# Performance work log

Hardware: AMD Instinct MI355X
Metric: run time of the kernel (lower is better)

## Reference

```python
import jax, jax.numpy as jnp
import numpy as np

TOPK = 8
EXTRA = 0  # ADDITIONAL_LAYERS_IN_GPU
CPU_TOPK = int(0.25 * 64)  # CPU_MOE_RATIO * num_experts = 16


def setup_inputs() -> dict:
    key = jax.random.key(0)
    k1, k2 = jax.random.split(key)
    hidden_states = jax.random.normal(k1, (4, 4096, 4096), dtype=jnp.float32)
    wg_weight = jax.random.normal(k2, (64, 4096), dtype=jnp.float32) * 0.02
    return {"hidden_states": hidden_states, "wg_weight": wg_weight}


def reference(hidden_states, wg_weight):
    bsz, seq_len, hidden_size = hidden_states.shape
    x = hidden_states.reshape(-1, hidden_size).astype(jnp.float32)  # [T, H]
    logits = jnp.einsum('th,eh->te', x, wg_weight)  # [T, 64]
    gates = jax.nn.softmax(logits, axis=1)
    values_all, indices_all = jax.lax.top_k(gates, TOPK + EXTRA)
    expert_weight = values_all[:, :TOPK]
    expert_index = indices_all[:, :TOPK]
    _, cpu_expert_index = jax.lax.top_k(gates, CPU_TOPK)
    cpu_expert_index = cpu_expert_index[:, 8 + EXTRA:]
    # norm_topk_prob=True, topk > 1
    eps = jnp.finfo(jnp.float32).eps
    denom = jnp.maximum(expert_weight.sum(axis=1, keepdims=True), eps)
    expert_weight = expert_weight / denom
    return (expert_weight, expert_index, cpu_expert_index, indices_all)
```

## Files before the change

### kernel.cpp

```cpp
#include <hip/hip_runtime.h>

#define T_TOK 16384
#define HDIM  4096
#define NEXP  64
#define TAU   2e-4f
#define BM    128

typedef unsigned short u16;
typedef u16   u16x8  __attribute__((ext_vector_type(8)));
typedef __bf16 bf16x8 __attribute__((ext_vector_type(8)));
typedef float f32x4  __attribute__((ext_vector_type(4)));

__device__ __forceinline__ void gld16(const void* g, void* l) {
    __builtin_amdgcn_global_load_lds(
        (const __attribute__((address_space(1))) void*)g,
        (__attribute__((address_space(3))) void*)l, 16, 0, 0);
}

__global__ __launch_bounds__(256)
void wsplit_kernel(const float* __restrict__ w, u16x8* __restrict__ wfrag,
                   float4* __restrict__ wt4, int* __restrict__ counter) {
    if (blockIdx.x == 0 && threadIdx.x == 0) counter[0] = 0;

    const int id  = blockIdx.x * 256 + threadIdx.x;
    const int e   = id >> 9;
    const int k8g = id & 511;
    const int k   = k8g * 8;

    const float* wp = w + (size_t)e * HDIM + k;
    const float4 v0 = *(const float4*)wp;
    const float4 v1 = *(const float4*)(wp + 4);

    wt4[(size_t)(2 * k8g) * NEXP + e]     = v0;
    wt4[(size_t)(2 * k8g + 1) * NEXP + e] = v1;

    const float fv[8] = {v0.x, v0.y, v0.z, v0.w, v1.x, v1.y, v1.z, v1.w};
    bf16x8 hv, lv;
#pragma unroll
    for (int j = 0; j < 8; ++j) {
        const __bf16 h = (__bf16)fv[j];
        hv[j] = h;
        lv[j] = (__bf16)(fv[j] - (float)h);
    }
    const int chunk = k >> 6;
    const int k8 = (k >> 3) & 7, ks = k8 >> 2, g = k8 & 3, nt = e >> 4;
    const int U = ks * 256 + nt * 64 + 16 * g + (e & 15);
    wfrag[(size_t)chunk * 1024 + U]       = __builtin_bit_cast(u16x8, hv);
    wfrag[(size_t)chunk * 1024 + 512 + U] = __builtin_bit_cast(u16x8, lv);
}

__global__ __launch_bounds__(256, 3)
void gate_gemm_mfma(const float* __restrict__ x, const u16x8* __restrict__ wfrag,
                    float* __restrict__ partial, int ksplit) {
    const int b      = blockIdx.x;
    const int kslice = b % ksplit;
    const int tblk   = b / ksplit;
    const int kspan  = HDIM / ksplit;
    const int k0     = kslice * kspan;
    const int t0     = tblk * BM;
    const int nch    = kspan >> 5;

    __shared__ __align__(16) unsigned char smem[48 * 1024];

    const int tid  = threadIdx.x;
    const int lane = tid & 63;
    const int wv   = tid >> 6;

    f32x4 acc[2][4];
#pragma unroll
    for (int m = 0; m < 2; ++m)
#pragma unroll
        for (int nt = 0; nt < 4; ++nt) acc[m][nt] = (f32x4){0.f, 0.f, 0.f, 0.f};

    auto stage = [&](int c, int p) {
        const int kc  = k0 + (c << 5);
        const u16x8* wsrc = wfrag + (size_t)(kc >> 6) * 1024 + ((c & 1) << 8);
        unsigned char* base = smem + (size_t)p * 1536 * 16;
        gld16(wsrc + tid,       base + (size_t)tid * 16);
        gld16(wsrc + 512 + tid, base + (size_t)(256 + tid) * 16);
#pragma unroll
        for (int j = 0; j < 4; ++j) {
            const int u   = tid + 256 * j;
            const int row = u >> 3;
            const int k4l = (u & 7) ^ (row & 7);
            gld16(x + (size_t)(t0 + row) * HDIM + kc + 4 * k4l,
                  base + (size_t)(512 + u) * 16);
        }
    };

    stage(0, 0);
    stage(1, 1);

    for (int c = 0; c < nch; ++c) {
        const int p = c & 1;

        if (c + 1 < nch) asm volatile("s_waitcnt vmcnt(6)" ::: "memory");
        else             asm volatile("s_waitcnt vmcnt(0)" ::: "memory");
        __builtin_amdgcn_sched_barrier(0);
        __builtin_amdgcn_s_barrier();
        __builtin_amdgcn_sched_barrier(0);

        const u16x8* wb = (const u16x8*)(smem + (size_t)p * 1536 * 16);
        const float* xb = (const float*)(smem + ((size_t)p * 1536 + 512) * 16);
        const int k8 = lane >> 4;

        bf16x8 axh[2], axl[2];
#pragma unroll
        for (int m = 0; m < 2; ++m) {
            const int row = (wv * 2 + m) * 16 + (lane & 15);
            const int p0  = row * 8 + ((2 * k8)     ^ (row & 7));
            const int p1  = row * 8 + ((2 * k8 + 1) ^ (row & 7));
            const float4 va = *(const float4*)(xb + 4 * p0);
            const float4 vb = *(const float4*)(xb + 4 * p1);
            const float fv[8] = {va.x, va.y, va.z, va.w, vb.x, vb.y, vb.z, vb.w};
            bf16x8 hv, lv;
#pragma unroll
            for (int j = 0; j < 8; ++j) {
                const __bf16 h = (__bf16)fv[j];
                hv[j] = h;
                lv[j] = (__bf16)(fv[j] - (float)h);
            }
            axh[m] = hv;
            axl[m] = lv;
        }
#pragma unroll
        for (int nt = 0; nt < 4; ++nt) {
            const bf16x8 bh = __builtin_bit_cast(bf16x8, wb[nt * 64 + lane]);
            const bf16x8 bl = __builtin_bit_cast(bf16x8, wb[256 + nt * 64 + lane]);
#pragma unroll
            for (int m = 0; m < 2; ++m) {
                acc[m][nt] = __builtin_amdgcn_mfma_f32_16x16x32_bf16(axh[m], bh, acc[m][nt], 0, 0, 0);
                acc[m][nt] = __builtin_amdgcn_mfma_f32_16x16x32_bf16(axh[m], bl, acc[m][nt], 0, 0, 0);
                acc[m][nt] = __builtin_amdgcn_mfma_f32_16x16x32_bf16(axl[m], bh, acc[m][nt], 0, 0, 0);
            }
        }

        __builtin_amdgcn_sched_barrier(0);
        __builtin_amdgcn_s_barrier();
        __builtin_amdgcn_sched_barrier(0);
        if (c + 2 < nch) stage(c + 2, p);
    }

    float* op = partial + (size_t)kslice * T_TOK * NEXP;
    const int ecol = lane & 15;
#pragma unroll
    for (int m = 0; m < 2; ++m) {
        const int trow = t0 + (wv * 2 + m) * 16 + ((lane >> 4) << 2);
#pragma unroll
        for (int nt = 0; nt < 4; ++nt)
#pragma unroll
            for (int r = 0; r < 4; ++r)
                op[(size_t)(trow + r) * NEXP + nt * 16 + ecol] = acc[m][nt][r];
    }
}

__global__ __launch_bounds__(256)
void gate_topk_f32(const float* __restrict__ partial, int ksplit,
                   float* __restrict__ out, int* __restrict__ list,
                   int* __restrict__ counter) {
    const int wave = threadIdx.x >> 6;
    const int lane = threadIdx.x & 63;
    const int t = blockIdx.x * 4 + wave;

    float l = 0.f;
    for (int s = 0; s < ksplit; ++s)
        l += partial[(size_t)s * T_TOK * NEXP + (size_t)t * NEXP + lane];

    float v = l;
    const int idx = lane;
    float myval = -3.4e38f;
    int   myidx = 0;
#pragma unroll
    for (int r = 0; r < 17; ++r) {
        float bv = v;
        int   bi = idx;
#pragma unroll
        for (int s = 1; s < 64; s <<= 1) {
            const float ov = __shfl_xor(bv, s);
            const int   oi = __shfl_xor(bi, s);
            if (ov > bv || (ov == bv && oi < bi)) { bv = ov; bi = oi; }
        }
        if (lane == r) { myval = bv; myidx = bi; }
        if (idx == bi) v = -3.4e38f;
    }

    const float nxt = __shfl(myval, (lane + 1) & 63);
    const bool close = (lane < 16) && (myval - nxt < TAU);
    if (__ballot(close) != 0ull) {
        if (lane == 0) { const int p = atomicAdd(counter, 1); list[p] = t; }
    }

    const float m = __shfl(myval, 0);
    const float p = (lane < 16) ? expf(myval - m) : 0.f;
    float s8 = (lane < 8) ? p : 0.f;
#pragma unroll
    for (int s = 1; s < 64; s <<= 1) s8 += __shfl_xor(s8, s);

    float* ew = out;
    float* ei = out + (size_t)T_TOK * 8;
    float* ci = out + (size_t)2 * T_TOK * 8;
    float* ia = out + (size_t)3 * T_TOK * 8;
    if (lane < 8) {
        ew[(size_t)t * 8 + lane] = p / s8;
        ei[(size_t)t * 8 + lane] = (float)myidx;
        ia[(size_t)t * 8 + lane] = (float)myidx;
    } else if (lane < 16) {
        ci[(size_t)t * 8 + (lane - 8)] = (float)myidx;
    }
}

__global__ __launch_bounds__(256)
void repair_partial(const float* __restrict__ x, const float4* __restrict__ wt4,
                    const int* __restrict__ list, const int* __restrict__ counter,
                    double* __restrict__ fpart) {
    const int lane = threadIdx.x & 63;
    const int wid  = (int)((blockIdx.x * blockDim.x + threadIdx.x) >> 6);
    const int nw   = (int)((gridDim.x * blockDim.x) >> 6);
    const int nit  = counter[0] * 16;

    for (int it = wid; it < nit; it += nw) {
        const int li = it >> 4;
        const int ks = it & 15;
        const int t  = __builtin_amdgcn_readfirstlane(list[li]);
        const float4* xr4 = (const float4*)(x + (size_t)t * HDIM) + ks * 64;
        const float4* wb  = wt4 + (size_t)ks * 64 * NEXP;

        double a0 = 0.0, a1 = 0.0, a2 = 0.0, a3 = 0.0;
#pragma unroll 4
        for (int j = 0; j < 64; j += 4) {
            const float4 w0 = wb[(size_t)(j + 0) * NEXP + lane];
            const float4 w1 = wb[(size_t)(j + 1) * NEXP + lane];
            const float4 w2 = wb[(size_t)(j + 2) * NEXP + lane];
            const float4 w3 = wb[(size_t)(j + 3) * NEXP + lane];
            const float4 x0 = xr4[j + 0];
            const float4 x1 = xr4[j + 1];
            const float4 x2 = xr4[j + 2];
            const float4 x3 = xr4[j + 3];
            a0 = fma((double)x0.x, (double)w0.x, a0);
            a0 = fma((double)x0.y, (double)w0.y, a0);
            a0 = fma((double)x0.z, (double)w0.z, a0);
            a0 = fma((double)x0.w, (double)w0.w, a0);
            a1 = fma((double)x1.x, (double)w1.x, a1);
            a1 = fma((double)x1.y, (double)w1.y, a1);
            a1 = fma((double)x1.z, (double)w1.z, a1);
            a1 = fma((double)x1.w, (double)w1.w, a1);
            a2 = fma((double)x2.x, (double)w2.x, a2);
            a2 = fma((double)x2.y, (double)w2.y, a2);
            a2 = fma((double)x2.z, (double)w2.z, a2);
            a2 = fma((double)x2.w, (double)w2.w, a2);
            a3 = fma((double)x3.x, (double)w3.x, a3);
            a3 = fma((double)x3.y, (double)w3.y, a3);
            a3 = fma((double)x3.z, (double)w3.z, a3);
            a3 = fma((double)x3.w, (double)w3.w, a3);
        }
        fpart[(size_t)li * 1024 + ks * 64 + lane] = (a0 + a1) + (a2 + a3);
    }
}

__global__ __launch_bounds__(256)
void repair_final(const double* __restrict__ fpart, const int* __restrict__ list,
                  const int* __restrict__ counter, float* __restrict__ out) {
    const int lane = threadIdx.x & 63;
    const int wid  = (int)((blockIdx.x * blockDim.x + threadIdx.x) >> 6);
    const int nw   = (int)((gridDim.x * blockDim.x) >> 6);
    const int n    = counter[0];

    for (int li = wid; li < n; li += nw) {
        const int t = __builtin_amdgcn_readfirstlane(list[li]);

        double v = 0.0;
#pragma unroll
        for (int ks = 0; ks < 16; ++ks)
            v += fpart[(size_t)li * 1024 + ks * 64 + lane];

        const int idx = lane;
        double mylog = -1.0e308;
        int    myidx = 0;
#pragma unroll
        for (int r = 0; r < 16; ++r) {
            double bv = v;
            int    bi = idx;
#pragma unroll
            for (int s = 1; s < 64; s <<= 1) {
                const double ov = __shfl_xor(bv, s);
                const int    oi = __shfl_xor(bi, s);
                if (ov > bv || (ov == bv && oi < bi)) { bv = ov; bi = oi; }
            }
            if (lane == r) { mylog = bv; myidx = bi; }
            if (idx == bi) v = -1.0e308;
        }

        const double m = __shfl(mylog, 0);
        const float p = (lane < 16) ? expf((float)(mylog - m)) : 0.f;
        float s8 = (lane < 8) ? p : 0.f;
#pragma unroll
        for (int s = 1; s < 64; s <<= 1) s8 += __shfl_xor(s8, s);

        float* ew = out;
        float* ei = out + (size_t)T_TOK * 8;
        float* ci = out + (size_t)2 * T_TOK * 8;
        float* ia = out + (size_t)3 * T_TOK * 8;
        if (lane < 8) {
            ew[(size_t)t * 8 + lane] = p / s8;
            ei[(size_t)t * 8 + lane] = (float)myidx;
            ia[(size_t)t * 8 + lane] = (float)myidx;
        } else if (lane < 16) {
            ci[(size_t)t * 8 + (lane - 8)] = (float)myidx;
        }
    }
}

extern "C" void kernel_launch(void* const* d_in, const int* in_sizes, int n_in,
                              void* d_out, int out_size, void* d_ws, size_t ws_size,
                              hipStream_t stream) {
    const float* x = (const float*)d_in[0];
    const float* w = (const float*)d_in[1];
    float* out     = (float*)d_out;

    const size_t slice      = (size_t)T_TOK * NEXP * sizeof(float);
    const size_t wfragBytes = (size_t)64 * 1024 * 16;
    const size_t wt4Bytes   = (size_t)NEXP * HDIM * sizeof(float);
    const size_t fpartBytes = (size_t)T_TOK * 16 * NEXP * sizeof(double);
    const size_t extra      = wfragBytes + wt4Bytes + fpartBytes +
                              (size_t)T_TOK * sizeof(int) + 64;

    int ksplit = 1;
    if      (ws_size >= 4 * slice + extra) ksplit = 4;
    else if (ws_size >= 2 * slice + extra) ksplit = 2;

    float*  partial = (float*)d_ws;
    u16x8*  wfrag   = (u16x8*)((char*)d_ws + (size_t)ksplit * slice);
    float4* wt4     = (float4*)((char*)wfrag + wfragBytes);
    double* fpart   = (double*)((char*)wt4 + wt4Bytes);
    int*    list    = (int*)((char*)fpart + fpartBytes);
    int*    counter = list + T_TOK;

    wsplit_kernel<<<128, 256, 0, stream>>>(w, wfrag, wt4, counter);
    gate_gemm_mfma<<<ksplit * (T_TOK / BM), 256, 0, stream>>>(x, wfrag, partial, ksplit);
    gate_topk_f32<<<T_TOK / 4, 256, 0, stream>>>(partial, ksplit, out, list, counter);
    repair_partial<<<4096, 256, 0, stream>>>(x, wt4, list, counter, fpart);
    repair_final<<<1024, 256, 0, stream>>>(fpart, list, counter, out);
}
```

Before: 160.0 us.

## Fuse fp64 repair passes into one per-token kernel driven by flags

Replaces the atomic-counter token list and the two-stage fp64 repair (partial sums to global, then a final reduce) with a per-token flag array and a single kernel that launches one block per token. Unflagged tokens exit immediately, while flagged ones do a 4-wave K-split fp64 dot product, reduce it in shared memory and redo the top-k. This removes the atomics, the large fp64 partial buffer and one launch. In exchange it launches 16384 blocks that mostly exit early, and each flagged token's work now sits on one CU instead of being spread across the grid.

Measured after the change: 214.3 us. +34.0%, slower.

```diff
diff --git a/kernel.cpp b/kernel.cpp
--- a/kernel.cpp
+++ b/kernel.cpp
@@ -19,9 +19,7 @@
 
 __global__ __launch_bounds__(256)
 void wsplit_kernel(const float* __restrict__ w, u16x8* __restrict__ wfrag,
-                   float4* __restrict__ wt4, int* __restrict__ counter) {
-    if (blockIdx.x == 0 && threadIdx.x == 0) counter[0] = 0;
-
+                   float4* __restrict__ wt4) {
     const int id  = blockIdx.x * 256 + threadIdx.x;
     const int e   = id >> 9;
     const int k8g = id & 511;
@@ -156,8 +154,7 @@
 
 __global__ __launch_bounds__(256)
 void gate_topk_f32(const float* __restrict__ partial, int ksplit,
-                   float* __restrict__ out, int* __restrict__ list,
-                   int* __restrict__ counter) {
+                   float* __restrict__ out, int* __restrict__ flags) {
     const int wave = threadIdx.x >> 6;
     const int lane = threadIdx.x & 63;
     const int t = blockIdx.x * 4 + wave;
@@ -186,9 +183,8 @@
 
     const float nxt = __shfl(myval, (lane + 1) & 63);
     const bool close = (lane < 16) && (myval - nxt < TAU);
-    if (__ballot(close) != 0ull) {
-        if (lane == 0) { const int p = atomicAdd(counter, 1); list[p] = t; }
-    }
+    const unsigned long long bal = __ballot(close);
+    if (lane == 0) flags[t] = (bal != 0ull) ? 1 : 0;
 
     const float m = __shfl(myval, 0);
     const float p = (lane < 16) ? expf(myval - m) : 0.f;
@@ -210,103 +206,87 @@
 }
 
 __global__ __launch_bounds__(256)
-void repair_partial(const float* __restrict__ x, const float4* __restrict__ wt4,
-                    const int* __restrict__ list, const int* __restrict__ counter,
-                    double* __restrict__ fpart) {
+void gate_repair_f64(const float* __restrict__ x, const float4* __restrict__ wt4,
+                     const int* __restrict__ flags, float* __restrict__ out) {
+    const int t = blockIdx.x;
+    if (flags[t] == 0) return;
+
+    __shared__ double part[4][NEXP];
+
+    const int wvs  = threadIdx.x >> 6;
     const int lane = threadIdx.x & 63;
-    const int wid  = (int)((blockIdx.x * blockDim.x + threadIdx.x) >> 6);
-    const int nw   = (int)((gridDim.x * blockDim.x) >> 6);
-    const int nit  = counter[0] * 16;
-
-    for (int it = wid; it < nit; it += nw) {
-        const int li = it >> 4;
-        const int ks = it & 15;
-        const int t  = __builtin_amdgcn_readfirstlane(list[li]);
-        const float4* xr4 = (const float4*)(x + (size_t)t * HDIM) + ks * 64;
-        const float4* wb  = wt4 + (size_t)ks * 64 * NEXP;
-
-        double a0 = 0.0, a1 = 0.0, a2 = 0.0, a3 = 0.0;
+
+    const float4* xr4 = (const float4*)(x + (size_t)t * HDIM) + wvs * 256;
+    const float4* wb  = wt4 + (size_t)wvs * 256 * NEXP;
+
+    double a0 = 0.0, a1 = 0.0, a2 = 0.0, a3 = 0.0;
 #pragma unroll 4
-        for (int j = 0; j < 64; j += 4) {
-            const float4 w0 = wb[(size_t)(j + 0) * NEXP + lane];
-            const float4 w1 = wb[(size_t)(j + 1) * NEXP + lane];
-            const float4 w2 = wb[(size_t)(j + 2) * NEXP + lane];
-            const float4 w3 = wb[(size_t)(j + 3) * NEXP + lane];
-            const float4 x0 = xr4[j + 0];
-            const float4 x1 = xr4[j + 1];
-            const float4 x2 = xr4[j + 2];
-            const float4 x3 = xr4[j + 3];
-            a0 = fma((double)x0.x, (double)w0.x, a0);
-            a0 = fma((double)x0.y, (double)w0.y, a0);
-            a0 = fma((double)x0.z, (double)w0.z, a0);
-            a0 = fma((double)x0.w, (double)w0.w, a0);
-            a1 = fma((double)x1.x, (double)w1.x, a1);
-            a1 = fma((double)x1.y, (double)w1.y, a1);
-            a1 = fma((double)x1.z, (double)w1.z, a1);
-            a1 = fma((double)x1.w, (double)w1.w, a1);
-            a2 = fma((double)x2.x, (double)w2.x, a2);
-            a2 = fma((double)x2.y, (double)w2.y, a2);
-            a2 = fma((double)x2.z, (double)w2.z, a2);
-            a2 = fma((double)x2.w, (double)w2.w, a2);
-            a3 = fma((double)x3.x, (double)w3.x, a3);
-            a3 = fma((double)x3.y, (double)w3.y, a3);
-            a3 = fma((double)x3.z, (double)w3.z, a3);
-            a3 = fma((double)x3.w, (double)w3.w, a3);
-        }
-        fpart[(size_t)li * 1024 + ks * 64 + lane] = (a0 + a1) + (a2 + a3);
-    }
-}
-
-__global__ __launch_bounds__(256)
-void repair_final(const double* __restrict__ fpart, const int* __restrict__ list,
-                  const int* __restrict__ counter, float* __restrict__ out) {
-    const int lane = threadIdx.x & 63;
-    const int wid  = (int)((blockIdx.x * blockDim.x + threadIdx.x) >> 6);
-    const int nw   = (int)((gridDim.x * blockDim.x) >> 6);
-    const int n    = counter[0];
-
-    for (int li = wid; li < n; li += nw) {
-        const int t = __builtin_amdgcn_readfirstlane(list[li]);
-
-        double v = 0.0;
-#pragma unroll
-        for (int ks = 0; ks < 16; ++ks)
-            v += fpart[(size_t)li * 1024 + ks * 64 + lane];
-
-        const int idx = lane;
-        double mylog = -1.0e308;
-        int    myidx = 0;
-#pragma unroll
-        for (int r = 0; r < 16; ++r) {
-            double bv = v;
-            int    bi = idx;
-#pragma unroll
-            for (int s = 1; s < 64; s <<= 1) {
-                const double ov = __shfl_xor(bv, s);
-                const int    oi = __shfl_xor(bi, s);
-                if (ov > bv || (ov == bv && oi < bi)) { bv = ov; bi = oi; }
-            }
-            if (lane == r) { mylog = bv; myidx = bi; }
-            if (idx == bi) v = -1.0e308;
-        }
-
-        const double m = __shfl(mylog, 0);
-        const float p = (lane < 16) ? expf((float)(mylog - m)) : 0.f;
-        float s8 = (lane < 8) ? p : 0.f;
-#pragma unroll
-        for (int s = 1; s < 64; s <<= 1) s8 += __shfl_xor(s8, s);
-
-        float* ew = out;
-        float* ei = out + (size_t)T_TOK * 8;
-        float* ci = out + (size_t)2 * T_TOK * 8;
-        float* ia = out + (size_t)3 * T_TOK * 8;
-        if (lane < 8) {
-            ew[(size_t)t * 8 + lane] = p / s8;
-            ei[(size_t)t * 8 + lane] = (float)myidx;
-            ia[(size_t)t * 8 + lane] = (float)myidx;
-        } else if (lane < 16) {
-            ci[(size_t)t * 8 + (lane - 8)] = (float)myidx;
-        }
+    for (int j = 0; j < 256; j += 4) {
+        const float4 w0 = wb[(size_t)(j + 0) * NEXP + lane];
+        const float4 w1 = wb[(size_t)(j + 1) * NEXP + lane];
+        const float4 w2 = wb[(size_t)(j + 2) * NEXP + lane];
+        const float4 w3 = wb[(size_t)(j + 3) * NEXP + lane];
+        const float4 x0 = xr4[j + 0];
+        const float4 x1 = xr4[j + 1];
+        const float4 x2 = xr4[j + 2];
+        const float4 x3 = xr4[j + 3];
+        a0 = fma((double)x0.x, (double)w0.x, a0);
+        a0 = fma((double)x0.y, (double)w0.y, a0);
+        a0 = fma((double)x0.z, (double)w0.z, a0);
+        a0 = fma((double)x0.w, (double)w0.w, a0);
+        a1 = fma((double)x1.x, (double)w1.x, a1);
+        a1 = fma((double)x1.y, (double)w1.y, a1);
+        a1 = fma((double)x1.z, (double)w1.z, a1);
+        a1 = fma((double)x1.w, (double)w1.w, a1);
+        a2 = fma((double)x2.x, (double)w2.x, a2);
+        a2 = fma((double)x2.y, (double)w2.y, a2);
+        a2 = fma((double)x2.z, (double)w2.z, a2);
+        a2 = fma((double)x2.w, (double)w2.w, a2);
+        a3 = fma((double)x3.x, (double)w3.x, a3);
+        a3 = fma((double)x3.y, (double)w3.y, a3);
+        a3 = fma((double)x3.z, (double)w3.z, a3);
+        a3 = fma((double)x3.w, (double)w3.w, a3);
+    }
+    part[wvs][lane] = (a0 + a1) + (a2 + a3);
+    __syncthreads();
+
+    if (wvs != 0) return;
+
+    double v = ((part[0][lane] + part[1][lane]) + (part[2][lane] + part[3][lane]));
+
+    const int idx = lane;
+    double mylog = -1.0e308;
+    int    myidx = 0;
+#pragma unroll
+    for (int r = 0; r < 16; ++r) {
+        double bv = v;
+        int    bi = idx;
+#pragma unroll
+        for (int s = 1; s < 64; s <<= 1) {
+            const double ov = __shfl_xor(bv, s);
+            const int    oi = __shfl_xor(bi, s);
+            if (ov > bv || (ov == bv && oi < bi)) { bv = ov; bi = oi; }
+        }
+        if (lane == r) { mylog = bv; myidx = bi; }
+        if (idx == bi) v = -1.0e308;
+    }
+
+    const double m = __shfl(mylog, 0);
+    const float p = (lane < 16) ? expf((float)(mylog - m)) : 0.f;
+    float s8 = (lane < 8) ? p : 0.f;
+#pragma unroll
+    for (int s = 1; s < 64; s <<= 1) s8 += __shfl_xor(s8, s);
+
+    float* ew = out;
+    float* ei = out + (size_t)T_TOK * 8;
+    float* ci = out + (size_t)2 * T_TOK * 8;
+    float* ia = out + (size_t)3 * T_TOK * 8;
+    if (lane < 8) {
+        ew[(size_t)t * 8 + lane] = p / s8;
+        ei[(size_t)t * 8 + lane] = (float)myidx;
+        ia[(size_t)t * 8 + lane] = (float)myidx;
+    } else if (lane < 16) {
+        ci[(size_t)t * 8 + (lane - 8)] = (float)myidx;
     }
 }
 
@@ -320,9 +300,7 @@
     const size_t slice      = (size_t)T_TOK * NEXP * sizeof(float);
     const size_t wfragBytes = (size_t)64 * 1024 * 16;
     const size_t wt4Bytes   = (size_t)NEXP * HDIM * sizeof(float);
-    const size_t fpartBytes = (size_t)T_TOK * 16 * NEXP * sizeof(double);
-    const size_t extra      = wfragBytes + wt4Bytes + fpartBytes +
-                              (size_t)T_TOK * sizeof(int) + 64;
+    const size_t extra      = wfragBytes + wt4Bytes + (size_t)T_TOK * sizeof(int);
 
     int ksplit = 1;
     if      (ws_size >= 4 * slice + extra) ksplit = 4;
@@ -331,13 +309,10 @@
     float*  partial = (float*)d_ws;
     u16x8*  wfrag   = (u16x8*)((char*)d_ws + (size_t)ksplit * slice);
     float4* wt4     = (float4*)((char*)wfrag + wfragBytes);
-    double* fpart   = (double*)((char*)wt4 + wt4Bytes);
-    int*    list    = (int*)((char*)fpart + fpartBytes);
-    int*    counter = list + T_TOK;
-
-    wsplit_kernel<<<128, 256, 0, stream>>>(w, wfrag, wt4, counter);
+    int*    flags   = (int*)((char*)wt4 + wt4Bytes);
+
+    wsplit_kernel<<<128, 256, 0, stream>>>(w, wfrag, wt4);
     gate_gemm_mfma<<<ksplit * (T_TOK / BM), 256, 0, stream>>>(x, wfrag, partial, ksplit);
-    gate_topk_f32<<<T_TOK / 4, 256, 0, stream>>>(partial, ksplit, out, list, counter);
-    repair_partial<<<4096, 256, 0, stream>>>(x, wt4, list, counter, fpart);
-    repair_final<<<1024, 256, 0, stream>>>(fpart, list, counter, out);
-}
+    gate_topk_f32<<<T_TOK / 4, 256, 0, stream>>>(partial, ksplit, out, flags);
+    gate_repair_f64<<<T_TOK, 256, 0, stream>>>(x, wt4, flags, out);
+}
```
